# Performance work log

Measured on AMD Instinct MI355X. Metric: run time of the kernel, lower is better.

The kernel has to match this reference:

```python
import jax, jax.numpy as jnp
import numpy as np

N_EMBD = 512
N_HEAD = 8
EPS = 1e-5


def setup_inputs() -> dict:
    key = jax.random.key(0)
    ks = jax.random.split(key, 8)
    C = N_EMBD
    s = lambda k, shape, fan: jax.random.normal(k, shape, jnp.float32) * (1.0 / np.sqrt(fan))
    return {
        "x": jax.random.normal(ks[0], (2, 4096, C), jnp.float32),
        "w_qkv": s(ks[1], (C, 3 * C), C), "b_qkv": jnp.zeros((3 * C,), jnp.float32),
        "w_attn_proj": s(ks[2], (C, C), C), "b_attn_proj": jnp.zeros((C,), jnp.float32),
        "w_fc": s(ks[3], (C, 4 * C), C), "b_fc": jnp.zeros((4 * C,), jnp.float32),
        "w_mlp_proj": s(ks[4], (4 * C, C), 4 * C), "b_mlp_proj": jnp.zeros((C,), jnp.float32),
        "ln1_g": jnp.ones((C,), jnp.float32), "ln1_b": jnp.zeros((C,), jnp.float32),
        "ln2_g": jnp.ones((C,), jnp.float32), "ln2_b": jnp.zeros((C,), jnp.float32),
    }


def _layernorm(x, g, b):
    mu = jnp.mean(x, axis=-1, keepdims=True)
    var = jnp.mean(jnp.square(x - mu), axis=-1, keepdims=True)
    return (x - mu) * jax.lax.rsqrt(var + EPS) * g + b


def _attention(x, w_qkv, b_qkv, w_proj, b_proj):
    B, T, C = x.shape
    hd = C // N_HEAD
    qkv = x @ w_qkv + b_qkv  # [B,T,3C]
    q, k, v = jnp.split(qkv, 3, axis=-1)
    q = q.reshape(B, T, N_HEAD, hd)
    k = k.reshape(B, T, N_HEAD, hd)
    v = v.reshape(B, T, N_HEAD, hd)
    # NOTE: faithful to source -- scale by sqrt(C) (n_embd), not sqrt(head_dim)
    scores = jnp.einsum('bthd,bshd->bhts', q, k) / jnp.sqrt(jnp.float32(C))
    mask = jnp.tril(jnp.ones((T, T), bool))
    scores = jnp.where(mask, scores, -jnp.inf)
    attn = jax.nn.softmax(scores, axis=-1)  # [B,H,T,T]
    y = jnp.einsum('bhts,bshd->bthd', attn, v).reshape(B, T, C)
    return y @ w_proj + b_proj


def _mlp(x, w_fc, b_fc, w_proj, b_proj):
    h = jax.nn.gelu(x @ w_fc + b_fc, approximate=True)
    return h @ w_proj + b_proj


def reference(x, w_qkv, b_qkv, w_attn_proj, b_attn_proj, w_fc, b_fc,
              w_mlp_proj, b_mlp_proj, ln1_g, ln1_b, ln2_g, ln2_b):
    x = x + _attention(_layernorm(x, ln1_g, ln1_b), w_qkv, b_qkv, w_attn_proj, b_attn_proj)
    x = x + _mlp(_layernorm(x, ln2_g, ln2_b), w_fc, b_fc, w_mlp_proj, b_mlp_proj)
    return x
```

## Files before the change

kernel.cpp:

```cpp
#include <hip/hip_runtime.h>
#include <hip/hip_bf16.h>
#include <math.h>

constexpr int B_ = 2;
constexpr int T_ = 4096;
constexpr int C_ = 512;
constexpr int H_ = 8;
constexpr int BT_ = B_ * T_;
constexpr float EPS_ = 1e-5f;

typedef __attribute__((ext_vector_type(8))) short bf16x8;
typedef __attribute__((ext_vector_type(4))) short short4v;
typedef __attribute__((ext_vector_type(8))) short short8v;
typedef __attribute__((ext_vector_type(4))) float f32x4;

__device__ __forceinline__ short f2bf(float f) {
    unsigned int u = __float_as_uint(f);
    unsigned int r = (u + 0x7fffu + ((u >> 16) & 1u)) >> 16;
    return (short)r;
}
__device__ __forceinline__ float bf2f(short s) {
    return __uint_as_float(((unsigned)(unsigned short)s) << 16);
}
__device__ __forceinline__ short f2bf_h(float f) {
    union { __hip_bfloat16 h; short s; } u;
    u.h = __float2bfloat16(f);
    return u.s;
}
__device__ __forceinline__ float exp2_f(float x) {
    float r;
    asm("v_exp_f32 %0, %1" : "=v"(r) : "v"(x));
    return r;
}

__device__ __forceinline__ float gelu_f(float v) {
    const float k0 = 0.7978845608028654f;
    const float k1 = 0.044715f;
    return 0.5f * v * (1.0f + tanhf(k0 * (v + k1 * v * v * v)));
}

__device__ __forceinline__ void gl_lds16(const short* gsrc, short* lds) {
    __builtin_amdgcn_global_load_lds(
        (const __attribute__((address_space(1))) void*)gsrc,
        (__attribute__((address_space(3))) void*)lds, 16, 0, 0);
}

__global__ __launch_bounds__(256) void transpose_w4(
    const float* __restrict__ W0, short* __restrict__ D0,
    const float* __restrict__ W1, short* __restrict__ D1,
    const float* __restrict__ W2, short* __restrict__ D2,
    const float* __restrict__ W3, short* __restrict__ D3) {
    __shared__ float tile[32][33];
    int bid = blockIdx.x;
    const float* W; short* D; int K, N, nx;
    if (bid < 768)       {             W = W0; D = D0; K = 512;  N = 1536; nx = 48; }
    else if (bid < 1024) { bid -= 768;  W = W1; D = D1; K = 512;  N = 512;  nx = 16; }
    else if (bid < 2048) { bid -= 1024; W = W2; D = D2; K = 512;  N = 2048; nx = 64; }
    else                 { bid -= 2048; W = W3; D = D3; K = 2048; N = 512;  nx = 16; }
    const int n0 = (bid % nx) * 32, k0 = (bid / nx) * 32;
    const int tx = threadIdx.x & 31, ty = threadIdx.x >> 5;
    #pragma unroll
    for (int j = 0; j < 4; j++)
        tile[ty + j * 8][tx] = W[(size_t)(k0 + ty + j * 8) * N + n0 + tx];
    __syncthreads();
    #pragma unroll
    for (int j = 0; j < 4; j++)
        D[(size_t)(n0 + ty + j * 8) * K + k0 + tx] = f2bf(tile[tx][ty + j * 8]);
}

__global__ __launch_bounds__(256) void transpose_v(const short* __restrict__ qkv,
                                                   short* __restrict__ Vt) {
    __shared__ short tile[64 * 72];
    const int tt = blockIdx.x, h = blockIdx.y, b = blockIdx.z;
    const int t = threadIdx.x;
    const int r = t >> 2, ch = (t & 3) * 16;
    const short* src = qkv + ((size_t)(b * T_ + tt * 64 + r)) * 1536 + 1024 + h * 64 + ch;
    *(short8v*)&tile[r * 72 + ch]     = *(const short8v*)src;
    *(short8v*)&tile[r * 72 + ch + 8] = *(const short8v*)(src + 8);
    __syncthreads();
    const int d = t >> 2, kc = (t & 3) * 16;
    short out[16];
    #pragma unroll
    for (int j = 0; j < 16; j++) {
        const int kvp = kc + j;
        const int K5 = kvp >> 5, w5 = kvp & 31;
        const int gg = (w5 >> 3) & 3, mm = (w5 >> 2) & 1, rr = w5 & 3;
        const int kv = K5 * 32 + 16 * mm + 4 * gg + rr;
        out[j] = tile[kv * 72 + d];
    }
    short* dst = Vt + ((size_t)((b * H_ + h) * 64 + d)) * T_ + tt * 64 + kc;
    *(short8v*)dst       = *(short8v*)&out[0];
    *(short8v*)(dst + 8) = *(short8v*)&out[8];
}

__global__ __launch_bounds__(256) void ln_bf16(const float* __restrict__ x,
                                               const float* __restrict__ g,
                                               const float* __restrict__ b,
                                               short* __restrict__ out) {
    const int row = blockIdx.x * 4 + (threadIdx.x >> 6);
    const int lane = threadIdx.x & 63;
    const float* xr = x + (size_t)row * C_;

    float4 v0 = *(const float4*)(xr + lane * 8);
    float4 v1 = *(const float4*)(xr + lane * 8 + 4);

    float s  = v0.x + v0.y + v0.z + v0.w + v1.x + v1.y + v1.z + v1.w;
    float s2 = v0.x*v0.x + v0.y*v0.y + v0.z*v0.z + v0.w*v0.w
             + v1.x*v1.x + v1.y*v1.y + v1.z*v1.z + v1.w*v1.w;
    #pragma unroll
    for (int off = 32; off; off >>= 1) {
        s  += __shfl_down(s, off);
        s2 += __shfl_down(s2, off);
    }
    s  = __shfl(s, 0);
    s2 = __shfl(s2, 0);

    const float mu  = s * (1.0f / C_);
    const float var = s2 * (1.0f / C_) - mu * mu;
    const float rs  = rsqrtf(var + EPS_);

    float4 g0 = *(const float4*)(g + lane * 8);
    float4 g1 = *(const float4*)(g + lane * 8 + 4);
    float4 b0 = *(const float4*)(b + lane * 8);
    float4 b1 = *(const float4*)(b + lane * 8 + 4);

    short8v o;
    o[0] = f2bf((v0.x - mu) * rs * g0.x + b0.x);
    o[1] = f2bf((v0.y - mu) * rs * g0.y + b0.y);
    o[2] = f2bf((v0.z - mu) * rs * g0.z + b0.z);
    o[3] = f2bf((v0.w - mu) * rs * g0.w + b0.w);
    o[4] = f2bf((v1.x - mu) * rs * g1.x + b1.x);
    o[5] = f2bf((v1.y - mu) * rs * g1.y + b1.y);
    o[6] = f2bf((v1.z - mu) * rs * g1.z + b1.z);
    o[7] = f2bf((v1.w - mu) * rs * g1.w + b1.w);
    *(short8v*)(out + (size_t)row * C_ + lane * 8) = o;
}

template<int BM, int ACT, int OUTBF16, int HASRES>
__global__ __launch_bounds__(256) void gemm_bf16(const short* __restrict__ A,
                                                 const short* __restrict__ Wt,
                                                 const float* __restrict__ bias,
                                                 const float* __restrict__ res,
                                                 void* __restrict__ outp,
                                                 int M, int N, int K,
                                                 int GX, int CY) {
    constexpr int MT = BM / 32;
    __shared__ short As[2][BM * 32];
    __shared__ short Bs[2][128 * 32];

    const int bid = blockIdx.x;
    const int xcd = bid & 7, jb = bid >> 3;
    const int by = xcd * CY + jb / GX;
    const int bx = jb % GX;

    const int t = threadIdx.x;
    const int w = t >> 6;
    const int l = t & 63;
    const int c = l & 15;
    const int g = l >> 4;
    const int wr = w >> 1, wc = w & 1;
    const int m0 = by * BM, n0 = bx * 128;

    const int r   = t >> 2;
    const int sch = ((t & 3) ^ (r & 3) ^ ((r >> 2) & 3)) * 8;
    const short* Asrc0 = A  + (size_t)(m0 + r) * K + sch;
    const short* Bsrc0 = Wt + (size_t)(n0 + r) * K + sch;
    const short* Bsrc1 = Wt + (size_t)(n0 + r + 64) * K + sch;
    const short* Asrc1 = (BM == 128) ? (A + (size_t)(m0 + r + 64) * K + sch) : nullptr;

    const int slot = ((g ^ (c & 3) ^ ((c >> 2) & 3))) * 8;

    auto stage = [&](int bb, int kt) {
        gl_lds16(Asrc0 + kt, &As[bb][w * 512]);
        if constexpr (BM == 128) gl_lds16(Asrc1 + kt, &As[bb][2048 + w * 512]);
        gl_lds16(Bsrc0 + kt, &Bs[bb][w * 512]);
        gl_lds16(Bsrc1 + kt, &Bs[bb][2048 + w * 512]);
    };

    f32x4 acc[MT][4] = {};

    stage(0, 0);
    asm volatile("s_waitcnt vmcnt(0)" ::: "memory");
    __syncthreads();
    int cur = 0;

    for (int kt = 0; kt < K; kt += 32) {
        if (kt + 32 < K) stage(cur ^ 1, kt + 32);

        bf16x8 af[MT], bfr[4];
        #pragma unroll
        for (int mt = 0; mt < MT; mt++)
            af[mt] = *(const bf16x8*)&As[cur][(wr * (BM / 2) + mt * 16 + c) * 32 + slot];
        #pragma unroll
        for (int nt = 0; nt < 4; nt++)
            bfr[nt] = *(const bf16x8*)&Bs[cur][(wc * 64 + nt * 16 + c) * 32 + slot];

        #pragma unroll
        for (int mt = 0; mt < MT; mt++)
            #pragma unroll
            for (int nt = 0; nt < 4; nt++)
                acc[mt][nt] = __builtin_amdgcn_mfma_f32_16x16x32_bf16(
                    af[mt], bfr[nt], acc[mt][nt], 0, 0, 0);

        asm volatile("s_waitcnt vmcnt(0)" ::: "memory");
        __syncthreads();
        cur ^= 1;
    }

    const int colb = n0 + wc * 64;
    float bias_v[4];
    #pragma unroll
    for (int nt = 0; nt < 4; nt++) bias_v[nt] = bias[colb + nt * 16 + c];

    float* out_f = (float*)outp;
    short* out_h = (short*)outp;

    #pragma unroll
    for (int mt = 0; mt < MT; mt++) {
        #pragma unroll
        for (int rr = 0; rr < 4; rr++) {
            const size_t row = (size_t)(m0 + wr * (BM / 2) + mt * 16 + 4 * g + rr);
            #pragma unroll
            for (int nt = 0; nt < 4; nt++) {
                const int col = colb + nt * 16 + c;
                float v = acc[mt][nt][rr] + bias_v[nt];
                if (ACT) v = gelu_f(v);
                if (HASRES) v += res[row * N + col];
                if (OUTBF16) out_h[row * N + col] = f2bf(v);
                else         out_f[row * N + col] = v;
            }
        }
    }
}

__global__ __launch_bounds__(256) void attn_mfma(const short* __restrict__ qkv,
                                                 const short* __restrict__ Vt,
                                                 short* __restrict__ y) {
    __shared__ union {
        struct { short K[2][64 * 64]; short V[2][64 * 64]; } s;
        float O[4][16][68];
    } sm;

    const int bid = blockIdx.x;
    const int xcd = bid & 7, jj = bid >> 3;
    const int lo = jj >> 6;
    const int qtr = jj & 63;
    const int qt = (qtr < 32) ? (63 - qtr) : (qtr - 32);
    const int g16 = xcd * 2 + lo;
    const int b = g16 >> 3, h = g16 & 7;

    const int tid = threadIdx.x, w = tid >> 6, lid = tid & 63;
    const int c = lid & 15, g = lid >> 4;
    const size_t base = (size_t)b * T_;
    const int bh = g16;

    const float qmul = 0.04419417382415922f * 1.4426950408889634f;

    bf16x8 qf0, qf1;
    {
        const short* qa = qkv + (base + qt * 64 + w * 16 + c) * 1536 + h * 64 + g * 8;
        bf16x8 a0 = *(const bf16x8*)qa;
        bf16x8 a1 = *(const bf16x8*)(qa + 32);
        #pragma unroll
        for (int i = 0; i < 8; i++) {
            qf0[i] = f2bf_h(bf2f(a0[i]) * qmul);
            qf1[i] = f2bf_h(bf2f(a1[i]) * qmul);
        }
    }

    const f32x4 kZero = {0.f, 0.f, 0.f, 0.f};
    bf16x8 kOnes;
    #pragma unroll
    for (int i = 0; i < 8; i++) kOnes[i] = (short)0x3F80;

    f32x4 ot[4] = {};
    f32x4 lacc = {0.f, 0.f, 0.f, 0.f};
    const int qg = qt * 64 + w * 16 + c;

    const int sr = tid >> 3;
    const int sc = ((tid & 7) ^ (sr & 7)) * 8;

    auto stage = [&](short* Kb, short* Vb, int st) {
        const short* ks = qkv + (base + st * 64 + sr) * 1536 + 512 + h * 64 + sc;
        const short* vs = Vt + ((size_t)(bh * 64 + sr)) * T_ + st * 64 + sc;
        gl_lds16(ks, Kb + w * 512);
        gl_lds16(ks + (size_t)32 * 1536, Kb + 2048 + w * 512);
        gl_lds16(vs, Vb + w * 512);
        gl_lds16(vs + (size_t)32 * T_, Vb + 2048 + w * 512);
    };

    const int rx = c & 7;
    const int ck0 = g ^ rx;
    const int ck1 = ck0 ^ 4;

    auto tile = [&](const short* Kb, const short* Vb, bool mask_diag) {
        f32x4 s[4];
        __builtin_amdgcn_s_setprio(1);
        #pragma unroll
        for (int mt = 0; mt < 4; mt++) {
            const short* krow = Kb + (mt * 16 + c) * 64;
            bf16x8 k0 = *(const bf16x8*)&krow[ck0 * 8];
            bf16x8 k1 = *(const bf16x8*)&krow[ck1 * 8];
            f32x4 z = __builtin_amdgcn_mfma_f32_16x16x32_bf16(k0, qf0, kZero, 0, 0, 0);
            s[mt] = __builtin_amdgcn_mfma_f32_16x16x32_bf16(k1, qf1, z, 0, 0, 0);
        }
        __builtin_amdgcn_s_setprio(0);

        float p[4][4];
        #pragma unroll
        for (int mt = 0; mt < 4; mt++)
            #pragma unroll
            for (int rr = 0; rr < 4; rr++) {
                float v = s[mt][rr];
                if (mask_diag && (qt * 64 + mt * 16 + 4 * g + rr > qg)) v = -1e30f;
                p[mt][rr] = exp2_f(v);
            }

        bf16x8 pb0, pb1;
        #pragma unroll
        for (int i = 0; i < 8; i++) {
            pb0[i] = f2bf_h(p[(i >> 2)][i & 3]);
            pb1[i] = f2bf_h(p[2 + (i >> 2)][i & 3]);
        }
        __builtin_amdgcn_s_setprio(1);
        lacc = __builtin_amdgcn_mfma_f32_16x16x32_bf16(kOnes, pb0, lacc, 0, 0, 0);
        lacc = __builtin_amdgcn_mfma_f32_16x16x32_bf16(kOnes, pb1, lacc, 0, 0, 0);
        #pragma unroll
        for (int dt = 0; dt < 4; dt++) {
            const short* vrow = Vb + (16 * dt + c) * 64;
            bf16x8 va0 = *(const bf16x8*)&vrow[ck0 * 8];
            bf16x8 va1 = *(const bf16x8*)&vrow[ck1 * 8];
            ot[dt] = __builtin_amdgcn_mfma_f32_16x16x32_bf16(va0, pb0, ot[dt], 0, 0, 0);
            ot[dt] = __builtin_amdgcn_mfma_f32_16x16x32_bf16(va1, pb1, ot[dt], 0, 0, 0);
        }
        __builtin_amdgcn_s_setprio(0);
    };

    short* K0 = sm.s.K[0]; short* K1 = sm.s.K[1];
    short* V0 = sm.s.V[0]; short* V1 = sm.s.V[1];

    stage(K0, V0, 0);
    asm volatile("s_waitcnt vmcnt(0)" ::: "memory");
    __syncthreads();

    int st = 0;
    while (st + 2 <= qt) {
        stage(K1, V1, st + 1);
        tile(K0, V0, false);
        asm volatile("s_waitcnt vmcnt(0)" ::: "memory");
        __syncthreads();
        stage(K0, V0, st + 2);
        tile(K1, V1, false);
        asm volatile("s_waitcnt vmcnt(0)" ::: "memory");
        __syncthreads();
        st += 2;
    }
    if (st < qt) {
        stage(K1, V1, st + 1);
        tile(K0, V0, false);
        asm volatile("s_waitcnt vmcnt(0)" ::: "memory");
        __syncthreads();
        tile(K1, V1, true);
    } else {
        tile(K0, V0, true);
    }
    __syncthreads();

    const float inv = 1.0f / lacc[0];
    #pragma unroll
    for (int dt = 0; dt < 4; dt++)
        #pragma unroll
        for (int rr = 0; rr < 4; rr++)
            sm.O[w][c][16 * dt + 4 * g + rr] = ot[dt][rr] * inv;
    const int q = lid >> 2, ch = lid & 3;
    short* dst = y + (base + qt * 64 + w * 16 + q) * 512 + h * 64 + ch * 16;
    short8v o0, o1;
    #pragma unroll
    for (int j = 0; j < 8; j++) o0[j] = f2bf(sm.O[w][q][ch * 16 + j]);
    #pragma unroll
    for (int j = 0; j < 8; j++) o1[j] = f2bf(sm.O[w][q][ch * 16 + 8 + j]);
    *(short8v*)dst = o0;
    *(short8v*)(dst + 8) = o1;
}

extern "C" void kernel_launch(void* const* d_in, const int* in_sizes, int n_in,
                              void* d_out, int out_size, void* d_ws, size_t ws_size,
                              hipStream_t stream) {
    const float* x           = (const float*)d_in[0];
    const float* w_qkv       = (const float*)d_in[1];
    const float* b_qkv       = (const float*)d_in[2];
    const float* w_attn_proj = (const float*)d_in[3];
    const float* b_attn_proj = (const float*)d_in[4];
    const float* w_fc        = (const float*)d_in[5];
    const float* b_fc        = (const float*)d_in[6];
    const float* w_mlp_proj  = (const float*)d_in[7];
    const float* b_mlp_proj  = (const float*)d_in[8];
    const float* ln1_g       = (const float*)d_in[9];
    const float* ln1_b       = (const float*)d_in[10];
    const float* ln2_g       = (const float*)d_in[11];
    const float* ln2_b       = (const float*)d_in[12];

    float* out = (float*)d_out;
    short* ws16 = (short*)d_ws;

    short* wqkvT = ws16;
    short* waT   = wqkvT + 1536 * 512;
    short* wfcT  = waT   + 512 * 512;
    short* wmT   = wfcT  + 2048 * 512;
    short* xn    = wmT   + 512 * 2048;
    short* ybuf  = xn    + (size_t)BT_ * 512;
    short* qkvh  = ybuf  + (size_t)BT_ * 512;
    short* vtb   = qkvh  + (size_t)BT_ * 2048;

    transpose_w4<<<3072, 256, 0, stream>>>(w_qkv, wqkvT, w_attn_proj, waT,
                                           w_fc, wfcT, w_mlp_proj, wmT);

    ln_bf16<<<BT_ / 4, 256, 0, stream>>>(x, ln1_g, ln1_b, xn);

    gemm_bf16<128, 0, 1, 0><<<12 * 64, 256, 0, stream>>>(
        xn, wqkvT, b_qkv, nullptr, qkvh, BT_, 1536, 512, 12, 8);

    transpose_v<<<dim3(T_ / 64, H_, B_), 256, 0, stream>>>(qkvh, vtb);

    attn_mfma<<<1024, 256, 0, stream>>>(qkvh, vtb, ybuf);

    gemm_bf16<64, 0, 0, 1><<<4 * 128, 256, 0, stream>>>(
        ybuf, waT, b_attn_proj, x, out, BT_, 512, 512, 4, 16);

    ln_bf16<<<BT_ / 4, 256, 0, stream>>>(out, ln2_g, ln2_b, xn);

    gemm_bf16<128, 1, 1, 0><<<16 * 64, 256, 0, stream>>>(
        xn, wfcT, b_fc, nullptr, qkvh, BT_, 2048, 512, 16, 8);

    gemm_bf16<64, 0, 0, 1><<<4 * 128, 256, 0, stream>>>(
        qkvh, wmT, b_mlp_proj, out, out, BT_, 512, 2048, 4, 16);
}
```

Baseline: 194.5 us.

## Triple-buffer GEMM LDS staging with counted vmcnt waits

Moves the bf16 GEMM from double to triple buffering of its A/B tiles in shared memory, prefetching two K-steps ahead. Each iteration waits only until the older stage's global-to-LDS loads have landed (partial vmcnt) instead of draining all outstanding loads, so memory latency overlaps more with MFMA work. This uses 1.5x the LDS per block, which may reduce occupancy. It also relies on hand-counted vmcnt values that must match the number of loads issued per stage.

```diff
diff --git a/kernel.cpp b/kernel.cpp
--- a/kernel.cpp
+++ b/kernel.cpp
@@ -145,8 +145,8 @@
                                                  int M, int N, int K,
                                                  int GX, int CY) {
     constexpr int MT = BM / 32;
-    __shared__ short As[2][BM * 32];
-    __shared__ short Bs[2][128 * 32];
+    __shared__ short As[3][BM * 32];
+    __shared__ short Bs[3][128 * 32];
 
     const int bid = blockIdx.x;
     const int xcd = bid & 7, jb = bid >> 3;
@@ -176,24 +176,35 @@
         gl_lds16(Bsrc0 + kt, &Bs[bb][w * 512]);
         gl_lds16(Bsrc1 + kt, &Bs[bb][2048 + w * 512]);
     };
+    auto wait_counted = [&]() {
+        if constexpr (BM == 128)
+            asm volatile("s_waitcnt vmcnt(4) lgkmcnt(0)" ::: "memory");
+        else
+            asm volatile("s_waitcnt vmcnt(3) lgkmcnt(0)" ::: "memory");
+    };
 
     f32x4 acc[MT][4] = {};
 
     stage(0, 0);
-    asm volatile("s_waitcnt vmcnt(0)" ::: "memory");
-    __syncthreads();
-    int cur = 0;
-
+    stage(1, 32);
+    wait_counted();
+    __builtin_amdgcn_s_barrier();
+
+    int bi = 0;
     for (int kt = 0; kt < K; kt += 32) {
-        if (kt + 32 < K) stage(cur ^ 1, kt + 32);
+        const bool pre = (kt + 64 < K);
+        if (pre) {
+            int b2 = bi + 2; if (b2 >= 3) b2 -= 3;
+            stage(b2, kt + 64);
+        }
 
         bf16x8 af[MT], bfr[4];
         #pragma unroll
         for (int mt = 0; mt < MT; mt++)
-            af[mt] = *(const bf16x8*)&As[cur][(wr * (BM / 2) + mt * 16 + c) * 32 + slot];
+            af[mt] = *(const bf16x8*)&As[bi][(wr * (BM / 2) + mt * 16 + c) * 32 + slot];
         #pragma unroll
         for (int nt = 0; nt < 4; nt++)
-            bfr[nt] = *(const bf16x8*)&Bs[cur][(wc * 64 + nt * 16 + c) * 32 + slot];
+            bfr[nt] = *(const bf16x8*)&Bs[bi][(wc * 64 + nt * 16 + c) * 32 + slot];
 
         #pragma unroll
         for (int mt = 0; mt < MT; mt++)
@@ -202,9 +213,10 @@
                 acc[mt][nt] = __builtin_amdgcn_mfma_f32_16x16x32_bf16(
                     af[mt], bfr[nt], acc[mt][nt], 0, 0, 0);
 
-        asm volatile("s_waitcnt vmcnt(0)" ::: "memory");
-        __syncthreads();
-        cur ^= 1;
+        if (pre) wait_counted();
+        else     asm volatile("s_waitcnt vmcnt(0) lgkmcnt(0)" ::: "memory");
+        __builtin_amdgcn_s_barrier();
+        bi = bi + 1; if (bi >= 3) bi = 0;
     }
 
     const int colb = n0 + wc * 64;
```

Result: slower. 199.1 us (+2.4%).
